# Kernel optimization log

Hardware: AMD Instinct MI355X
Metric: run time of the kernel (lower is better)

Reference implementation:

```python
import jax, jax.numpy as jnp
import numpy as np

BINS = 10
LOSS_WEIGHT = 1.0
EDGE_TOP = 1.0 + 1e-6  # edges[-1] += 1e-6 in the torch module


def setup_inputs() -> dict:
    key = jax.random.key(0)
    k1, k2, k3 = jax.random.split(key, 3)
    shape = (32, 1048576)
    # pred: sigmoid probabilities in [0, 1)
    pred = jax.random.uniform(k1, shape, dtype=jnp.float32)
    target = (jax.random.uniform(k2, shape) < 0.3).astype(jnp.float32)
    label_weight = (jax.random.uniform(k3, shape) < 0.95).astype(jnp.float32)
    return {"pred": pred, "target": target, "label_weight": label_weight}


def reference(pred, target, label_weight):
    p = pred.reshape(-1)
    t = target.reshape(-1).astype(p.dtype)
    lw = label_weight.reshape(-1).astype(p.dtype)

    I = jnp.sum(p * t)                       # intersection
    S = jnp.sum(p) + jnp.sum(t)              # denominator of Dice

    # gradient norm proxy: |2I/S * pred.detach() - target| (no grad flows through g)
    g = jax.lax.stop_gradient(jnp.abs(2.0 * I / S * p - t))

    valid = lw > 0
    tot = jnp.maximum(jnp.sum(valid.astype(p.dtype)), 1.0)

    # bin assignment: edges are i/bins for i=0..bins, with edges[-1] bumped by 1e-6,
    # so g in [i/bins, (i+1)/bins) -> bin i, and g in [1, 1+1e-6) -> bin bins-1.
    in_range = valid & (g < EDGE_TOP)
    bin_idx = jnp.clip(jnp.floor(g * BINS).astype(jnp.int32), 0, BINS - 1)

    # one-pass histogram of valid, in-range elements
    counts = jnp.zeros(BINS, dtype=p.dtype).at[bin_idx].add(in_range.astype(p.dtype))
    n_nonempty = jnp.sum(counts > 0).astype(p.dtype)

    # weight = tot / num_in_bin for elements in a non-empty bin, else 0; then /n
    per_elem = jnp.where(in_range, tot / jnp.maximum(counts[bin_idx], 1.0), 0.0)
    weights = per_elem / jnp.maximum(n_nonempty, 1.0)

    loss = 1.0 - jnp.sum(2.0 * p * t * weights) / S
    return loss * LOSS_WEIGHT
```

## Files before the change

kernel.cpp:

```cpp
#include <hip/hip_runtime.h>


constexpr int BINS = 10;
constexpr int NB1  = 2048;
constexpr int NB2  = 2048;
constexpr int OFF1 = 64;
constexpr int OFF2 = 16384;

__global__ __launch_bounds__(256) void k_reduce1(const float4* __restrict__ p,
                                                 const float4* __restrict__ t,
                                                 float* __restrict__ ws,
                                                 int n4, int n) {
    int idx    = blockIdx.x * blockDim.x + threadIdx.x;
    int stride = gridDim.x * blockDim.x;
    float sI = 0.f, sP = 0.f, sT = 0.f;
#pragma unroll 4
    for (int i = idx; i < n4; i += stride) {
        float4 pv = p[i];
        float4 tv = t[i];
        sI += pv.x * tv.x + pv.y * tv.y + pv.z * tv.z + pv.w * tv.w;
        sP += pv.x + pv.y + pv.z + pv.w;
        sT += tv.x + tv.y + tv.z + tv.w;
    }
    if (idx == 0) {
        const float* pf = (const float*)p;
        const float* tf = (const float*)t;
        for (int i = n4 * 4; i < n; ++i) { sI += pf[i] * tf[i]; sP += pf[i]; sT += tf[i]; }
    }
#pragma unroll
    for (int o = 32; o > 0; o >>= 1) {
        sI += __shfl_down(sI, o);
        sP += __shfl_down(sP, o);
        sT += __shfl_down(sT, o);
    }
    __shared__ float rI[4], rP[4], rT[4];
    int wave = threadIdx.x >> 6, lane = threadIdx.x & 63;
    if (lane == 0) { rI[wave] = sI; rP[wave] = sP; rT[wave] = sT; }
    __syncthreads();
    if (threadIdx.x == 0) {
        float* o = &ws[OFF1 + blockIdx.x * 4];
        o[0] = rI[0] + rI[1] + rI[2] + rI[3];
        o[1] = rP[0] + rP[1] + rP[2] + rP[3];
        o[2] = rT[0] + rT[1] + rT[2] + rT[3];
    }
}

__global__ __launch_bounds__(256) void k_mid(float* __restrict__ ws) {
    __shared__ float red[256];
    int tid = threadIdx.x;
    int q = tid & 3, idx = tid >> 2;
    float v = 0.f;
    if (q < 3)
        for (int b = idx; b < NB1; b += 64) v += ws[OFF1 + b * 4 + q];
    red[tid] = v;
    __syncthreads();
    if (tid < 3) {
        float s = 0.f;
        for (int i = 0; i < 64; ++i) s += red[i * 4 + tid];
        red[tid] = s;
    }
    __syncthreads();
    if (tid == 0) {
        float I = red[0];
        float S = red[1] + red[2];
        ws[0] = 2.f * I / S;
        ws[1] = S;
    }
}

__global__ __launch_bounds__(256) void k_pass2(const float4* __restrict__ p,
                                               const float4* __restrict__ t,
                                               const float4* __restrict__ lw,
                                               float* __restrict__ ws,
                                               int n4, int n) {
    const float scale    = ws[0];
    const float edge_top = 1.0f + 1e-6f;

    float cnt[BINS], sm[BINS];
#pragma unroll
    for (int b = 0; b < BINS; ++b) { cnt[b] = 0.f; sm[b] = 0.f; }
    float vcount = 0.f;

    int idx    = blockIdx.x * blockDim.x + threadIdx.x;
    int stride = gridDim.x * blockDim.x;

#pragma unroll 2
    for (int i = idx; i < n4; i += stride) {
        float4 pv = p[i], tv = t[i], wv = lw[i];
        float pj[4] = {pv.x, pv.y, pv.z, pv.w};
        float tj[4] = {tv.x, tv.y, tv.z, tv.w};
        float wj[4] = {wv.x, wv.y, wv.z, wv.w};
#pragma unroll
        for (int j = 0; j < 4; ++j) {
            bool valid = wj[j] > 0.f;
            vcount += valid ? 1.f : 0.f;
            float g = fabsf(scale * pj[j] - tj[j]);
            bool inr = valid && (g < edge_top);
            int b = (int)(g * 10.f);
            b = b > (BINS - 1) ? (BINS - 1) : b;
            float addc = inr ? 1.f : 0.f;
            float adds = inr ? 2.f * pj[j] * tj[j] : 0.f;
#pragma unroll
            for (int b0 = 0; b0 < BINS; ++b0) {
                bool m = (b == b0);
                cnt[b0] += m ? addc : 0.f;
                sm[b0]  += m ? adds : 0.f;
            }
        }
    }
    if (idx == 0) {
        const float* pf = (const float*)p;
        const float* tf = (const float*)t;
        const float* wf = (const float*)lw;
        for (int i = n4 * 4; i < n; ++i) {
            bool valid = wf[i] > 0.f;
            vcount += valid ? 1.f : 0.f;
            float g = fabsf(scale * pf[i] - tf[i]);
            bool inr = valid && (g < edge_top);
            int b = (int)(g * 10.f);
            b = b > (BINS - 1) ? (BINS - 1) : b;
            float addc = inr ? 1.f : 0.f;
            float adds = inr ? 2.f * pf[i] * tf[i] : 0.f;
#pragma unroll
            for (int b0 = 0; b0 < BINS; ++b0) {
                bool m = (b == b0);
                cnt[b0] += m ? addc : 0.f;
                sm[b0]  += m ? adds : 0.f;
            }
        }
    }

    __shared__ float red[256 * 21];
    float* mine = &red[threadIdx.x * 21];
#pragma unroll
    for (int b0 = 0; b0 < BINS; ++b0) { mine[b0] = cnt[b0]; mine[BINS + b0] = sm[b0]; }
    mine[2 * BINS] = vcount;
    __syncthreads();

    int tid = threadIdx.x;
    if (tid < 2 * BINS + 1) {
        float v = 0.f;
        for (int i = 0; i < 256; ++i) v += red[i * 21 + tid];
        ws[OFF2 + blockIdx.x * 32 + tid] = v;
    }
}

__global__ __launch_bounds__(256) void k_final(const float* __restrict__ ws,
                                               float* __restrict__ out) {
    __shared__ float red[256];
    __shared__ float fin[32];
    int tid  = threadIdx.x;
    int slot = tid & 31;
    int grp  = tid >> 5;
    float v = 0.f;
    if (slot < 2 * BINS + 1)
        for (int b = grp; b < NB2; b += 8) v += ws[OFF2 + b * 32 + slot];
    red[tid] = v;
    __syncthreads();
    if (tid < 32) {
        float s = 0.f;
#pragma unroll
        for (int g = 0; g < 8; ++g) s += red[g * 32 + tid];
        fin[tid] = s;
    }
    __syncthreads();
    if (tid == 0) {
        float S   = ws[1];
        float tot = fmaxf(fin[20], 1.0f);
        int nne = 0;
        for (int b = 0; b < BINS; ++b) nne += (fin[b] > 0.f) ? 1 : 0;
        float nn = fmaxf((float)nne, 1.0f);
        float wsum = 0.f;
        for (int b = 0; b < BINS; ++b) {
            float c = fmaxf(fin[b], 1.0f);
            wsum += fin[BINS + b] * (tot / c);
        }
        wsum /= nn;
        out[0] = 1.0f - wsum / S;
    }
}

extern "C" void kernel_launch(void* const* d_in, const int* in_sizes, int n_in,
                              void* d_out, int out_size, void* d_ws, size_t ws_size,
                              hipStream_t stream) {
    const float* p  = (const float*)d_in[0];
    const float* t  = (const float*)d_in[1];
    const float* lw = (const float*)d_in[2];
    float* ws  = (float*)d_ws;
    float* out = (float*)d_out;
    int n  = in_sizes[0];
    int n4 = n >> 2;

    k_reduce1<<<NB1, 256, 0, stream>>>((const float4*)p, (const float4*)t, ws, n4, n);
    k_mid<<<1, 256, 0, stream>>>(ws);
    k_pass2<<<NB2, 256, 0, stream>>>((const float4*)p, (const float4*)t,
                                     (const float4*)lw, ws, n4, n);
    k_final<<<1, 256, 0, stream>>>(ws, out);
}
```

Baseline: 473.3 us.

## Replace grid-stride loops with per-block chunks and batched up-front vector loads

Both streaming kernels drop the grid-stride loop over a fixed 2048-block grid. Each block now owns one contiguous chunk of 8 float4 per thread per input. Every thread issues all of its loads for that chunk before doing any arithmetic, which raises memory-level parallelism. The grid size is now computed from the input size, and the reduction kernels take the block count as a parameter with a tighter 24-float per-block stride for partials. In exchange there are more blocks and partials to reduce, and register use rises from holding 24 float4 values in the pass-2 kernel.

Measured after the change: 515.2 us. 8.9% more time.

```diff
diff --git a/kernel.cpp b/kernel.cpp
--- a/kernel.cpp
+++ b/kernel.cpp
@@ -2,30 +2,48 @@
 
 
 constexpr int BINS = 10;
-constexpr int NB1  = 2048;
-constexpr int NB2  = 2048;
+constexpr int K1   = 8;
+constexpr int K2   = 8;
+constexpr int CH1  = 256 * K1;
+constexpr int CH2  = 256 * K2;
 constexpr int OFF1 = 64;
-constexpr int OFF2 = 16384;
+constexpr int OFF2 = 16448;
 
 __global__ __launch_bounds__(256) void k_reduce1(const float4* __restrict__ p,
                                                  const float4* __restrict__ t,
                                                  float* __restrict__ ws,
                                                  int n4, int n) {
-    int idx    = blockIdx.x * blockDim.x + threadIdx.x;
-    int stride = gridDim.x * blockDim.x;
+    const int chunk = blockIdx.x * CH1;
+    const int base  = chunk + threadIdx.x;
     float sI = 0.f, sP = 0.f, sT = 0.f;
-#pragma unroll 4
-    for (int i = idx; i < n4; i += stride) {
-        float4 pv = p[i];
-        float4 tv = t[i];
-        sI += pv.x * tv.x + pv.y * tv.y + pv.z * tv.z + pv.w * tv.w;
-        sP += pv.x + pv.y + pv.z + pv.w;
-        sT += tv.x + tv.y + tv.z + tv.w;
-    }
-    if (idx == 0) {
-        const float* pf = (const float*)p;
-        const float* tf = (const float*)t;
-        for (int i = n4 * 4; i < n; ++i) { sI += pf[i] * tf[i]; sP += pf[i]; sT += tf[i]; }
+
+    if (chunk + CH1 <= n4) {
+        float4 pv[K1], tv[K1];
+#pragma unroll
+        for (int k = 0; k < K1; ++k) pv[k] = p[base + k * 256];
+#pragma unroll
+        for (int k = 0; k < K1; ++k) tv[k] = t[base + k * 256];
+#pragma unroll
+        for (int k = 0; k < K1; ++k) {
+            sI += pv[k].x * tv[k].x + pv[k].y * tv[k].y + pv[k].z * tv[k].z + pv[k].w * tv[k].w;
+            sP += pv[k].x + pv[k].y + pv[k].z + pv[k].w;
+            sT += tv[k].x + tv[k].y + tv[k].z + tv[k].w;
+        }
+    } else {
+        for (int k = 0; k < K1; ++k) {
+            int i = base + k * 256;
+            if (i < n4) {
+                float4 pv = p[i], tv = t[i];
+                sI += pv.x * tv.x + pv.y * tv.y + pv.z * tv.z + pv.w * tv.w;
+                sP += pv.x + pv.y + pv.z + pv.w;
+                sT += tv.x + tv.y + tv.z + tv.w;
+            }
+        }
+        if (blockIdx.x == gridDim.x - 1 && threadIdx.x == 0) {
+            const float* pf = (const float*)p;
+            const float* tf = (const float*)t;
+            for (int i = n4 * 4; i < n; ++i) { sI += pf[i] * tf[i]; sP += pf[i]; sT += tf[i]; }
+        }
     }
 #pragma unroll
     for (int o = 32; o > 0; o >>= 1) {
@@ -45,13 +63,13 @@
     }
 }
 
-__global__ __launch_bounds__(256) void k_mid(float* __restrict__ ws) {
+__global__ __launch_bounds__(256) void k_mid(float* __restrict__ ws, int nb1) {
     __shared__ float red[256];
     int tid = threadIdx.x;
-    int q = tid & 3, idx = tid >> 2;
+    int q = tid & 3, row = tid >> 2;
     float v = 0.f;
     if (q < 3)
-        for (int b = idx; b < NB1; b += 64) v += ws[OFF1 + b * 4 + q];
+        for (int b = row; b < nb1; b += 64) v += ws[OFF1 + b * 4 + q];
     red[tid] = v;
     __syncthreads();
     if (tid < 3) {
@@ -81,52 +99,57 @@
     for (int b = 0; b < BINS; ++b) { cnt[b] = 0.f; sm[b] = 0.f; }
     float vcount = 0.f;
 
-    int idx    = blockIdx.x * blockDim.x + threadIdx.x;
-    int stride = gridDim.x * blockDim.x;
-
-#pragma unroll 2
-    for (int i = idx; i < n4; i += stride) {
-        float4 pv = p[i], tv = t[i], wv = lw[i];
-        float pj[4] = {pv.x, pv.y, pv.z, pv.w};
-        float tj[4] = {tv.x, tv.y, tv.z, tv.w};
-        float wj[4] = {wv.x, wv.y, wv.z, wv.w};
-#pragma unroll
-        for (int j = 0; j < 4; ++j) {
-            bool valid = wj[j] > 0.f;
-            vcount += valid ? 1.f : 0.f;
-            float g = fabsf(scale * pj[j] - tj[j]);
-            bool inr = valid && (g < edge_top);
-            int b = (int)(g * 10.f);
-            b = b > (BINS - 1) ? (BINS - 1) : b;
-            float addc = inr ? 1.f : 0.f;
-            float adds = inr ? 2.f * pj[j] * tj[j] : 0.f;
-#pragma unroll
-            for (int b0 = 0; b0 < BINS; ++b0) {
-                bool m = (b == b0);
-                cnt[b0] += m ? addc : 0.f;
-                sm[b0]  += m ? adds : 0.f;
+    auto process = [&](float pe, float te, float we) {
+        bool valid = we > 0.f;
+        vcount += valid ? 1.f : 0.f;
+        float g = fabsf(scale * pe - te);
+        bool inr = valid && (g < edge_top);
+        int b = (int)(g * 10.f);
+        b = b > (BINS - 1) ? (BINS - 1) : b;
+        float addc = inr ? 1.f : 0.f;
+        float adds = inr ? 2.f * pe * te : 0.f;
+#pragma unroll
+        for (int b0 = 0; b0 < BINS; ++b0) {
+            bool m = (b == b0);
+            cnt[b0] += m ? addc : 0.f;
+            sm[b0]  += m ? adds : 0.f;
+        }
+    };
+
+    const int chunk = blockIdx.x * CH2;
+    const int base  = chunk + threadIdx.x;
+
+    if (chunk + CH2 <= n4) {
+        float4 pv[K2], tv[K2], wv[K2];
+#pragma unroll
+        for (int k = 0; k < K2; ++k) pv[k] = p[base + k * 256];
+#pragma unroll
+        for (int k = 0; k < K2; ++k) tv[k] = t[base + k * 256];
+#pragma unroll
+        for (int k = 0; k < K2; ++k) wv[k] = lw[base + k * 256];
+#pragma unroll
+        for (int k = 0; k < K2; ++k) {
+            process(pv[k].x, tv[k].x, wv[k].x);
+            process(pv[k].y, tv[k].y, wv[k].y);
+            process(pv[k].z, tv[k].z, wv[k].z);
+            process(pv[k].w, tv[k].w, wv[k].w);
+        }
+    } else {
+        for (int k = 0; k < K2; ++k) {
+            int i = base + k * 256;
+            if (i < n4) {
+                float4 pv = p[i], tv = t[i], wv = lw[i];
+                process(pv.x, tv.x, wv.x);
+                process(pv.y, tv.y, wv.y);
+                process(pv.z, tv.z, wv.z);
+                process(pv.w, tv.w, wv.w);
             }
         }
-    }
-    if (idx == 0) {
-        const float* pf = (const float*)p;
-        const float* tf = (const float*)t;
-        const float* wf = (const float*)lw;
-        for (int i = n4 * 4; i < n; ++i) {
-            bool valid = wf[i] > 0.f;
-            vcount += valid ? 1.f : 0.f;
-            float g = fabsf(scale * pf[i] - tf[i]);
-            bool inr = valid && (g < edge_top);
-            int b = (int)(g * 10.f);
-            b = b > (BINS - 1) ? (BINS - 1) : b;
-            float addc = inr ? 1.f : 0.f;
-            float adds = inr ? 2.f * pf[i] * tf[i] : 0.f;
-#pragma unroll
-            for (int b0 = 0; b0 < BINS; ++b0) {
-                bool m = (b == b0);
-                cnt[b0] += m ? addc : 0.f;
-                sm[b0]  += m ? adds : 0.f;
-            }
+        if (blockIdx.x == gridDim.x - 1 && threadIdx.x == 0) {
+            const float* pf = (const float*)p;
+            const float* tf = (const float*)t;
+            const float* wf = (const float*)lw;
+            for (int i = n4 * 4; i < n; ++i) process(pf[i], tf[i], wf[i]);
         }
     }
 
@@ -141,26 +164,26 @@
     if (tid < 2 * BINS + 1) {
         float v = 0.f;
         for (int i = 0; i < 256; ++i) v += red[i * 21 + tid];
-        ws[OFF2 + blockIdx.x * 32 + tid] = v;
+        ws[OFF2 + blockIdx.x * 24 + tid] = v;
     }
 }
 
 __global__ __launch_bounds__(256) void k_final(const float* __restrict__ ws,
-                                               float* __restrict__ out) {
+                                               float* __restrict__ out, int nb2) {
     __shared__ float red[256];
-    __shared__ float fin[32];
+    __shared__ float fin[24];
     int tid  = threadIdx.x;
-    int slot = tid & 31;
-    int grp  = tid >> 5;
+    int grp  = tid / 24;
+    int slot = tid - grp * 24;
     float v = 0.f;
-    if (slot < 2 * BINS + 1)
-        for (int b = grp; b < NB2; b += 8) v += ws[OFF2 + b * 32 + slot];
+    if (tid < 240 && slot <= 2 * BINS)
+        for (int b = grp; b < nb2; b += 10) v += ws[OFF2 + b * 24 + slot];
     red[tid] = v;
     __syncthreads();
-    if (tid < 32) {
+    if (tid <= 2 * BINS) {
         float s = 0.f;
 #pragma unroll
-        for (int g = 0; g < 8; ++g) s += red[g * 32 + tid];
+        for (int g = 0; g < 10; ++g) s += red[g * 24 + tid];
         fin[tid] = s;
     }
     __syncthreads();
@@ -191,9 +214,14 @@
     int n  = in_sizes[0];
     int n4 = n >> 2;
 
-    k_reduce1<<<NB1, 256, 0, stream>>>((const float4*)p, (const float4*)t, ws, n4, n);
-    k_mid<<<1, 256, 0, stream>>>(ws);
-    k_pass2<<<NB2, 256, 0, stream>>>((const float4*)p, (const float4*)t,
+    int nb1 = (n4 + CH1 - 1) / CH1;
+    int nb2 = (n4 + CH2 - 1) / CH2;
+    if (nb1 < 1) nb1 = 1;
+    if (nb2 < 1) nb2 = 1;
+
+    k_reduce1<<<nb1, 256, 0, stream>>>((const float4*)p, (const float4*)t, ws, n4, n);
+    k_mid<<<1, 256, 0, stream>>>(ws, nb1);
+    k_pass2<<<nb2, 256, 0, stream>>>((const float4*)p, (const float4*)t,
                                      (const float4*)lw, ws, n4, n);
-    k_final<<<1, 256, 0, stream>>>(ws, out);
-}
+    k_final<<<1, 256, 0, stream>>>(ws, out, nb2);
+}
```
